# Optimization experiments

Measured on AMD Instinct MI355X. Metric: run time of the kernel, lower is better.

The kernel has to match this reference:

```python
import jax, jax.numpy as jnp
import numpy as np

D_MODEL = 512
N_HEADS = 8
HEAD_DIM = D_MODEL // N_HEADS
ROPE_BASE = 10000.0


def _rope_cache(seq_len, dtype):
    half = HEAD_DIM // 2
    inv_freq = 1.0 / (ROPE_BASE ** (jnp.arange(half, dtype=dtype) / half))
    t = jnp.arange(seq_len, dtype=dtype)
    freqs = jnp.einsum('i,j->ij', t, inv_freq)            # [L, half]
    cos = jnp.repeat(jnp.cos(freqs), 2, axis=-1)          # [L, head_dim]
    sin = jnp.repeat(jnp.sin(freqs), 2, axis=-1)
    return cos[None, None], sin[None, None]               # [1,1,L,head_dim]


def _rotate_half(x):
    x_even = x[..., ::2]
    x_odd = x[..., 1::2]
    return jnp.stack([-x_odd, x_even], axis=-1).reshape(x.shape)


def setup_inputs() -> dict:
    key = jax.random.key(0)
    ks = jax.random.split(key, 10)
    B, Lq, Lkv, C = 2, 2048, 4096, D_MODEL
    s = 1.0 / np.sqrt(C)
    inp = {
        'q': jax.random.normal(ks[0], (B, Lq, C), jnp.float32),
        'kv': jax.random.normal(ks[1], (B, Lkv, C), jnp.float32),
        'Wq': jax.random.normal(ks[2], (C, C), jnp.float32) * s,
        'bq': jnp.zeros((C,), jnp.float32),
        'Wk': jax.random.normal(ks[3], (C, C), jnp.float32) * s,
        'bk': jnp.zeros((C,), jnp.float32),
        'Wv': jax.random.normal(ks[4], (C, C), jnp.float32) * s,
        'bv': jnp.zeros((C,), jnp.float32),
        'Wo': jax.random.normal(ks[5], (C, C), jnp.float32) * s,
        'bo': jnp.zeros((C,), jnp.float32),
    }
    return inp


def reference(q, kv, Wq, bq, Wk, bk, Wv, bv, Wo, bo):
    B, Lq, C = q.shape
    Lkv = kv.shape[1]
    H, Dh = N_HEADS, HEAD_DIM
    # projections (torch Linear: x @ W.T + b)
    qh = (q @ Wq.T + bq).reshape(B, Lq, H, Dh).transpose(0, 2, 1, 3)    # [B,H,Lq,Dh]
    kh = (kv @ Wk.T + bk).reshape(B, Lkv, H, Dh).transpose(0, 2, 1, 3)  # [B,H,Lkv,Dh]
    vh = (kv @ Wv.T + bv).reshape(B, Lkv, H, Dh).transpose(0, 2, 1, 3)
    # RoPE applied to K only
    cos, sin = _rope_cache(Lkv, kh.dtype)
    kh = kh * cos + _rotate_half(kh) * sin
    # manual softmax attention (full [B,H,Lq,Lkv] matrix, as in the source)
    scale = 1.0 / np.sqrt(Dh).astype(np.float32)
    attn = jnp.einsum('bhqd,bhkd->bhqk', qh, kh) * scale
    attn = jax.nn.softmax(attn, axis=-1)
    out = jnp.einsum('bhqk,bhkd->bhqd', attn, vh)
    out = out.transpose(0, 2, 1, 3).reshape(B, Lq, C)
    return out @ Wo.T + bo
```

## Files before the change

kernel.cpp:

```cpp
#include <hip/hip_runtime.h>
#include <math.h>

typedef _Float16 f16;
typedef __attribute__((ext_vector_type(8))) f16 f16x8;
typedef __attribute__((ext_vector_type(4))) float f32x4;
typedef __attribute__((ext_vector_type(4))) int   i32x4;

__device__ __forceinline__ short f2h(float f) {
    return __builtin_bit_cast(short, (f16)f);
}

__device__ __forceinline__ void gload16(const void* g, void* l) {
    __builtin_amdgcn_global_load_lds(
        (const __attribute__((address_space(1))) unsigned int*)g,
        (__attribute__((address_space(3))) unsigned int*)l, 16, 0, 0);
}

#define MFMA16(A, B, C) __builtin_amdgcn_mfma_f32_16x16x32_f16(A, B, C, 0, 0, 0)
#define EXP2(x) __builtin_amdgcn_exp2f(x)

__global__ __launch_bounds__(256) void convert_kernel(
    const float* __restrict__ q, const float* __restrict__ kv,
    const float* __restrict__ Wq, const float* __restrict__ Wk,
    const float* __restrict__ Wv, const float* __restrict__ Wo,
    short* __restrict__ cq, short* __restrict__ ckv,
    short* __restrict__ wq, short* __restrict__ wk,
    short* __restrict__ wv, short* __restrict__ wo)
{
    int g = blockIdx.x * 256 + threadIdx.x;
    const float* src; short* dst; int local;
    if      (g <  524288) { src = q;  dst = cq;  local = g; }
    else if (g < 1572864) { src = kv; dst = ckv; local = g -  524288; }
    else if (g < 1638400) { src = Wq; dst = wq;  local = g - 1572864; }
    else if (g < 1703936) { src = Wk; dst = wk;  local = g - 1638400; }
    else if (g < 1769472) { src = Wv; dst = wv;  local = g - 1703936; }
    else                  { src = Wo; dst = wo;  local = g - 1769472; }
    float4 v = *(const float4*)(src + (size_t)local * 4);
    short4 hv; short* hp = (short*)&hv;
    hp[0] = f2h(v.x); hp[1] = f2h(v.y); hp[2] = f2h(v.z); hp[3] = f2h(v.w);
    *(short4*)(dst + (size_t)local * 4) = hv;
}

template<int RT, int EP>
__device__ __forceinline__ void gemm_core(
    short* As, short* Bs,
    const short* __restrict__ X, const short* __restrict__ W,
    const float* __restrict__ bias, float scale,
    float* __restrict__ outF, short* __restrict__ outH,
    int m0, int n0)
{
    const int tid  = threadIdx.x;
    const int wave = tid >> 6, lane = tid & 63;
    const int quad = lane >> 4, col = lane & 15;
    const int wy = wave >> 1, wx = wave & 1;
    constexpr int MT  = RT / 32;
    constexpr int ASZ = RT * 32;

    f32x4 acc[MT][4];
    #pragma unroll
    for (int i = 0; i < MT; ++i)
        #pragma unroll
        for (int j = 0; j < 4; ++j) acc[i][j] = (f32x4){0.f, 0.f, 0.f, 0.f};

    int aoff[MT], boff[4];
    #pragma unroll
    for (int t = 0; t < MT; ++t)
        aoff[t] = (wy * (RT / 2) + t * 16 + col) * 32 + quad * 8;
    #pragma unroll
    for (int t = 0; t < 4; ++t)
        boff[t] = (wx * 64 + t * 16 + col) * 32 + quad * 8;

    const short* Abase = X + (size_t)m0 * 512;
    const short* Bbase = W + (size_t)n0 * 512;

#define STAGE_G(BUF, KB) {                                                   \
    _Pragma("unroll")                                                        \
    for (int i = 0; i < RT / 64; ++i) {                                      \
        int p = i * 256 + tid; int r = p >> 2, qq = p & 3;                   \
        gload16(Abase + (size_t)r * 512 + (KB) + qq * 8,                     \
                &As[(BUF) * ASZ + (i * 256 + wave * 64) * 8]);               \
    }                                                                        \
    _Pragma("unroll")                                                        \
    for (int i = 0; i < 2; ++i) {                                            \
        int p = i * 256 + tid; int r = p >> 2, qq = p & 3;                   \
        gload16(Bbase + (size_t)r * 512 + (KB) + qq * 8,                     \
                &Bs[(BUF) * 4096 + (i * 256 + wave * 64) * 8]);              \
    }                                                                        \
}

    STAGE_G(0, 0);
    asm volatile("s_waitcnt vmcnt(0)" ::: "memory");
    __syncthreads();

    for (int kb = 0; kb < 512; kb += 32) {
        const int cur = (kb >> 5) & 1;
        if (kb + 32 < 512) STAGE_G(cur ^ 1, kb + 32);
        f16x8 a[MT], b[4];
        #pragma unroll
        for (int t = 0; t < MT; ++t) a[t] = *(const f16x8*)&As[cur * ASZ + aoff[t]];
        #pragma unroll
        for (int t = 0; t < 4; ++t)  b[t] = *(const f16x8*)&Bs[cur * 4096 + boff[t]];
        #pragma unroll
        for (int tm = 0; tm < MT; ++tm)
            #pragma unroll
            for (int tn = 0; tn < 4; ++tn)
                acc[tm][tn] = MFMA16(a[tm], b[tn], acc[tm][tn]);
        asm volatile("s_waitcnt vmcnt(0)" ::: "memory");
        __syncthreads();
    }
#undef STAGE_G

    #pragma unroll
    for (int tn = 0; tn < 4; ++tn) {
        int ng = n0 + wx * 64 + tn * 16 + col;
        float bb = bias[ng];
        #pragma unroll
        for (int tm = 0; tm < MT; ++tm) {
            int mb = m0 + wy * (RT / 2) + tm * 16 + quad * 4;
            if constexpr (EP == 2) {
                int bb_ = mb >> 12, kvg = mb & 4095;
                int tile = kvg >> 7, kv128 = kvg & 127;
                int t01 = (kv128 >> 6) & 1, sv = (kv128 >> 4) & 3, qd = (kv128 >> 2) & 3;
                int hh = ng >> 6, dd = ng & 63, dt = dd >> 4, d15 = dd & 15;
                size_t base = ((((size_t)((bb_ * 8 + hh) * 32 + tile) * 16)
                               + sv * 4 + dt) * 64 + qd * 16 + d15) * 8 + t01 * 4;
                short4 s4; short* sp = (short*)&s4;
                #pragma unroll
                for (int r = 0; r < 4; ++r) sp[r] = f2h(acc[tm][tn][r] + bb);
                *(short4*)&outH[base] = s4;
            } else if constexpr (EP == 1) {
                #pragma unroll
                for (int r = 0; r < 4; ++r)
                    outH[(size_t)(mb + r) * 512 + ng] =
                        f2h((acc[tm][tn][r] + bb) * scale);
            } else {
                #pragma unroll
                for (int r = 0; r < 4; ++r)
                    outF[(size_t)(mb + r) * 512 + ng] = acc[tm][tn][r] + bb;
            }
        }
    }
}

__global__ __launch_bounds__(256) void fused_qkv_gemm_kernel(
    const short* __restrict__ cq, const short* __restrict__ ckv,
    const short* __restrict__ wq, const short* __restrict__ wk,
    const short* __restrict__ wv,
    const float* __restrict__ bq, const float* __restrict__ bk,
    const float* __restrict__ bv, float qscale,
    short* __restrict__ Qh, short* __restrict__ Kh, short* __restrict__ Vf)
{
    __shared__ short As[2 * 128 * 32], Bs[2 * 128 * 32];
    int bi = blockIdx.x;
    if (bi < 128) {
        gemm_core<128, 1>(As, Bs, cq, wq, bq, qscale, nullptr, Qh,
                          (bi >> 2) * 128, (bi & 3) * 128);
    } else if (bi < 384) {
        bi -= 128;
        gemm_core<128, 1>(As, Bs, ckv, wk, bk, 1.0f, nullptr, Kh,
                          (bi >> 2) * 128, (bi & 3) * 128);
    } else {
        bi -= 384;
        gemm_core<128, 2>(As, Bs, ckv, wv, bv, 1.0f, nullptr, Vf,
                          (bi >> 2) * 128, (bi & 3) * 128);
    }
}

__global__ __launch_bounds__(256) void gemm_o_kernel(
    const short* __restrict__ X, const short* __restrict__ W,
    const float* __restrict__ bias, float* __restrict__ outF)
{
    __shared__ short As[2 * 64 * 32], Bs[2 * 128 * 32];
    gemm_core<64, 0>(As, Bs, X, W, bias, 1.0f, outF, nullptr,
                     (int)(blockIdx.x >> 2) * 64, (int)(blockIdx.x & 3) * 128);
}

__global__ __launch_bounds__(256) void rope_kernel(short* __restrict__ Kh)
{
    __shared__ float2 tbl[4][32];
    const int t = threadIdx.x;
    const int g = blockIdx.x * 256 + t;
    if (t < 128) {
        int p = t >> 5, i = t & 31;
        int pos = (blockIdx.x * 4 + p) & 4095;
        float fr = expf((float)i * -0.28782313662425576f);
        float sv, cv;
        sincosf((float)pos * fr, &sv, &cv);
        tbl[p][i] = make_float2(cv, sv);
    }
    __syncthreads();

    int row = g >> 6;
    int c8  = (g & 63) * 8;
    size_t off = (size_t)row * 512 + c8;
    f16x8 hv = *(const f16x8*)&Kh[off];
    float x[8];
    #pragma unroll
    for (int j = 0; j < 8; ++j) x[j] = (float)hv[j];
    const int rl = row & 3;
    const int ib = (c8 & 63) >> 1;
    #pragma unroll
    for (int p = 0; p < 4; ++p) {
        float2 cs = tbl[rl][ib + p];
        float e = x[2 * p], o = x[2 * p + 1];
        x[2 * p]     = e * cs.x - o * cs.y;
        x[2 * p + 1] = o * cs.x + e * cs.y;
    }
    #pragma unroll
    for (int j = 0; j < 8; ++j) hv[j] = (f16)x[j];
    *(f16x8*)&Kh[off] = hv;
}

__global__ __launch_bounds__(256, 2) void attn_mfma_kernel(
    const short* __restrict__ Qh, const short* __restrict__ Kh,
    const short* __restrict__ Vfrag, short* __restrict__ AO)
{
    __shared__ char smem[17408];

    const int tid  = threadIdx.x;
    const int wave = tid >> 6;
    const int lane = tid & 63;
    const int quad = lane >> 4;
    const int l15  = lane & 15;

    const int bh = blockIdx.x & 15;
    const int qt = blockIdx.x >> 4;
    const int b  = bh >> 3, h = bh & 7;
    const int qb = qt * 32;

    f16x8 qf[2][2];
    #pragma unroll
    for (int tq = 0; tq < 2; ++tq)
        #pragma unroll
        for (int c = 0; c < 2; ++c)
            qf[tq][c] = *(const f16x8*)&Qh[((size_t)(b * 2048 + qb + tq * 16 + l15)) * 512
                                           + h * 64 + c * 32 + quad * 8];

    f32x4 o[2][4];
    f32x4 l4[2];
    #pragma unroll
    for (int i = 0; i < 2; ++i) {
        l4[i] = (f32x4){0.f, 0.f, 0.f, 0.f};
        #pragma unroll
        for (int j = 0; j < 4; ++j) o[i][j] = (f32x4){0.f, 0.f, 0.f, 0.f};
    }

    const f32x4 zero4 = (f32x4){0.f, 0.f, 0.f, 0.f};
    f16x8 vones;
    #pragma unroll
    for (int j = 0; j < 8; ++j) vones[j] = (f16)1.0f;

    const short* kp = Kh + ((size_t)(b * 4096 + wave * 16 + l15)) * 512
                      + h * 64 + quad * 8;
    const short* vbase = Vfrag + (size_t)(b * 8 + h) * 262144
                         + ((size_t)(wave * 4) * 64 + lane) * 8;

#define LDK(DST, I) { const short* _k = kp + (size_t)(I) * 65536;            \
    DST[0] = *(const f16x8*)(_k);                                            \
    DST[1] = *(const f16x8*)(_k + 32);                                       \
    DST[2] = *(const f16x8*)(_k + 32768);                                    \
    DST[3] = *(const f16x8*)(_k + 32800); }
#define LDV(DST, I) { const short* _v = vbase + (size_t)(I) * 8192;          \
    DST[0] = *(const f16x8*)(_v);                                            \
    DST[1] = *(const f16x8*)(_v + 512);                                      \
    DST[2] = *(const f16x8*)(_v + 1024);                                     \
    DST[3] = *(const f16x8*)(_v + 1536); }

#define QK(KC) {                                                             \
    __builtin_amdgcn_s_setprio(1);                                           \
    _Pragma("unroll")                                                        \
    for (int t = 0; t < 2; ++t) {                                            \
        s0[t] = MFMA16(KC[0], qf[t][0], zero4);                              \
        s0[t] = MFMA16(KC[1], qf[t][1], s0[t]);                              \
        s1[t] = MFMA16(KC[2], qf[t][0], zero4);                              \
        s1[t] = MFMA16(KC[3], qf[t][1], s1[t]);                              \
    }                                                                        \
    __builtin_amdgcn_s_setprio(0); }

#define FIN(VP) {                                                            \
    _Pragma("unroll")                                                        \
    for (int t = 0; t < 2; ++t) {                                            \
        float e0 = EXP2(s0[t][0]), e1 = EXP2(s0[t][1]);                      \
        float e2 = EXP2(s0[t][2]), e3 = EXP2(s0[t][3]);                      \
        float e4 = EXP2(s1[t][0]), e5 = EXP2(s1[t][1]);                      \
        float e6 = EXP2(s1[t][2]), e7 = EXP2(s1[t][3]);                      \
        i32x4 pw;                                                            \
        pw.x = __builtin_bit_cast(int, __builtin_amdgcn_cvt_pkrtz(e0, e1));  \
        pw.y = __builtin_bit_cast(int, __builtin_amdgcn_cvt_pkrtz(e2, e3));  \
        pw.z = __builtin_bit_cast(int, __builtin_amdgcn_cvt_pkrtz(e4, e5));  \
        pw.w = __builtin_bit_cast(int, __builtin_amdgcn_cvt_pkrtz(e6, e7));  \
        f16x8 p8 = __builtin_bit_cast(f16x8, pw);                            \
        __builtin_amdgcn_s_setprio(1);                                       \
        _Pragma("unroll")                                                    \
        for (int dt = 0; dt < 4; ++dt)                                       \
            o[t][dt] = MFMA16(p8, VP[dt], o[t][dt]);                         \
        l4[t] = MFMA16(p8, vones, l4[t]);                                    \
        __builtin_amdgcn_s_setprio(0);                                       \
    } }

    f16x8 kK[4], vV[4];
    f32x4 s0[2], s1[2];

    LDV(vV, 0);
    LDK(kK, 0);
    QK(kK);

    #pragma unroll 1
    for (int it = 1; it < 32; ++it) {
        LDK(kK, it);
        FIN(vV);
        LDV(vV, it);
        QK(kK);
    }
    FIN(vV);

#undef FIN
#undef QK
#undef LDV
#undef LDK

    float* Opart = (float*)smem;
    float* Lpart = (float*)(smem + 16896);

    float inv_save[4];
    #pragma unroll
    for (int pass = 0; pass < 2; ++pass) {
        if (pass) __syncthreads();
        #pragma unroll
        for (int tq = 0; tq < 2; ++tq)
            #pragma unroll
            for (int dh = 0; dh < 2; ++dh) {
                int dt = pass * 2 + dh;
                #pragma unroll
                for (int r = 0; r < 4; ++r)
                    Opart[wave * (32 * 33) + (tq * 16 + quad * 4 + r) * 33 + dh * 16 + l15] = o[tq][dt][r];
            }
        if (pass == 0 && l15 == 0) {
            #pragma unroll
            for (int tq = 0; tq < 2; ++tq)
                #pragma unroll
                for (int r = 0; r < 4; ++r)
                    Lpart[wave * 32 + tq * 16 + quad * 4 + r] = l4[tq][r];
        }
        __syncthreads();
        #pragma unroll
        for (int r = 0; r < 4; ++r) {
            int qq = wave * 8 + r * 2 + (lane >> 5);
            int d  = lane & 31;
            float v = Opart[0 * (32 * 33) + qq * 33 + d] + Opart[1 * (32 * 33) + qq * 33 + d]
                    + Opart[2 * (32 * 33) + qq * 33 + d] + Opart[3 * (32 * 33) + qq * 33 + d];
            float inv;
            if (pass == 0) {
                float l = Lpart[qq] + Lpart[32 + qq] + Lpart[64 + qq] + Lpart[96 + qq];
                inv = 1.0f / l;
                inv_save[r] = inv;
            } else {
                inv = inv_save[r];
            }
            float val = v * inv;
            size_t oo = ((size_t)(b * 2048 + qb + qq)) * 512 + h * 64 + pass * 32 + d;
            AO[oo] = f2h(val);
        }
    }
}

extern "C" void kernel_launch(void* const* d_in, const int* in_sizes, int n_in,
                              void* d_out, int out_size, void* d_ws, size_t ws_size,
                              hipStream_t stream) {
    const float* q  = (const float*)d_in[0];
    const float* kv = (const float*)d_in[1];
    const float* Wq = (const float*)d_in[2];
    const float* bq = (const float*)d_in[3];
    const float* Wk = (const float*)d_in[4];
    const float* bk = (const float*)d_in[5];
    const float* Wv = (const float*)d_in[6];
    const float* bv = (const float*)d_in[7];
    const float* Wo = (const float*)d_in[8];
    const float* bo = (const float*)d_in[9];
    float* out = (float*)d_out;

    char* ws = (char*)d_ws;
    const size_t MB = 1024 * 1024;
    short* cq  = (short*)(ws + 0 * MB);
    short* ckv = (short*)(ws + 4 * MB);
    short* wq  = (short*)(ws + 12 * MB);
    short* wk  = wq + 262144;
    short* wv  = wk + 262144;
    short* wo  = wv + 262144;
    short* Qh  = (short*)(ws + 14 * MB);
    short* Kh  = (short*)(ws + 18 * MB);
    short* Vf  = (short*)(ws + 26 * MB);
    short* AO  = (short*)(ws + 34 * MB);

    const float qscale = 0.18033688011112043f;

    dim3 blk(256);
    convert_kernel<<<7168, blk, 0, stream>>>(
        q, kv, Wq, Wk, Wv, Wo, cq, ckv, wq, wk, wv, wo);

    fused_qkv_gemm_kernel<<<640, blk, 0, stream>>>(
        cq, ckv, wq, wk, wv, bq, bk, bv, qscale, Qh, Kh, Vf);

    rope_kernel<<<2048, blk, 0, stream>>>(Kh);

    attn_mfma_kernel<<<1024, blk, 0, stream>>>(Qh, Kh, Vf, AO);

    gemm_o_kernel<<<256, blk, 0, stream>>>(AO, wo, bo, out);
}
```

Measured before the change: 197.3 us.

## Double-buffer K/V fragments, compute row sums in VALU, raise occupancy

The K and V register fragments are now double-buffered, so the loads for the next tile are issued a full iteration ahead of use, with the loop unrolled by two. The row-sum MFMA against a ones vector is replaced by scalar adds of the exponentials plus a cross-lane shuffle reduction, which removes one MFMA per tile. Launch bounds are raised to three blocks per SIMD pair to increase occupancy. The extra buffers raise register pressure, and the tighter register budget may cause spills.

```diff
diff --git a/kernel.cpp b/kernel.cpp
--- a/kernel.cpp
+++ b/kernel.cpp
@@ -211,7 +211,7 @@
     *(f16x8*)&Kh[off] = hv;
 }
 
-__global__ __launch_bounds__(256, 2) void attn_mfma_kernel(
+__global__ __launch_bounds__(256, 3) void attn_mfma_kernel(
     const short* __restrict__ Qh, const short* __restrict__ Kh,
     const short* __restrict__ Vfrag, short* __restrict__ AO)
 {
@@ -237,18 +237,13 @@
                                            + h * 64 + c * 32 + quad * 8];
 
     f32x4 o[2][4];
-    f32x4 l4[2];
-    #pragma unroll
-    for (int i = 0; i < 2; ++i) {
-        l4[i] = (f32x4){0.f, 0.f, 0.f, 0.f};
+    float lsum[2] = {0.f, 0.f};
+    #pragma unroll
+    for (int i = 0; i < 2; ++i)
         #pragma unroll
         for (int j = 0; j < 4; ++j) o[i][j] = (f32x4){0.f, 0.f, 0.f, 0.f};
-    }
 
     const f32x4 zero4 = (f32x4){0.f, 0.f, 0.f, 0.f};
-    f16x8 vones;
-    #pragma unroll
-    for (int j = 0; j < 8; ++j) vones[j] = (f16)1.0f;
 
     const short* kp = Kh + ((size_t)(b * 4096 + wave * 16 + l15)) * 512
                       + h * 64 + quad * 8;
@@ -284,6 +279,7 @@
         float e2 = EXP2(s0[t][2]), e3 = EXP2(s0[t][3]);                      \
         float e4 = EXP2(s1[t][0]), e5 = EXP2(s1[t][1]);                      \
         float e6 = EXP2(s1[t][2]), e7 = EXP2(s1[t][3]);                      \
+        lsum[t] += ((e0 + e1) + (e2 + e3)) + ((e4 + e5) + (e6 + e7));        \
         i32x4 pw;                                                            \
         pw.x = __builtin_bit_cast(int, __builtin_amdgcn_cvt_pkrtz(e0, e1));  \
         pw.y = __builtin_bit_cast(int, __builtin_amdgcn_cvt_pkrtz(e2, e3));  \
@@ -294,30 +290,40 @@
         _Pragma("unroll")                                                    \
         for (int dt = 0; dt < 4; ++dt)                                       \
             o[t][dt] = MFMA16(p8, VP[dt], o[t][dt]);                         \
-        l4[t] = MFMA16(p8, vones, l4[t]);                                    \
         __builtin_amdgcn_s_setprio(0);                                       \
     } }
 
-    f16x8 kK[4], vV[4];
+#define BODY(I, KC, KN, VP) {                                                \
+    LDK(KN, (I) + 1);                                                        \
+    FIN(VP);                                                                 \
+    LDV(VP, (I) + 1);                                                        \
+    QK(KC); }
+
+    f16x8 kA[4], kB[4], vA[4], vB[4];
     f32x4 s0[2], s1[2];
 
-    LDV(vV, 0);
-    LDK(kK, 0);
-    QK(kK);
+    LDK(kA, 0); LDV(vA, 0); LDK(kB, 1); LDV(vB, 1);
+    QK(kA);
 
     #pragma unroll 1
-    for (int it = 1; it < 32; ++it) {
-        LDK(kK, it);
-        FIN(vV);
-        LDV(vV, it);
-        QK(kK);
-    }
-    FIN(vV);
-
+    for (int j = 1; j < 31; j += 2) {
+        BODY(j,     kB, kA, vA);
+        BODY(j + 1, kA, kB, vB);
+    }
+    BODY(31, kB, kA, vA);
+    FIN(vB);
+
+#undef BODY
 #undef FIN
 #undef QK
 #undef LDV
 #undef LDK
+
+    #pragma unroll
+    for (int t = 0; t < 2; ++t) {
+        lsum[t] += __shfl_xor(lsum[t], 16);
+        lsum[t] += __shfl_xor(lsum[t], 32);
+    }
 
     float* Opart = (float*)smem;
     float* Lpart = (float*)(smem + 16896);
@@ -335,12 +341,9 @@
                 for (int r = 0; r < 4; ++r)
                     Opart[wave * (32 * 33) + (tq * 16 + quad * 4 + r) * 33 + dh * 16 + l15] = o[tq][dt][r];
             }
-        if (pass == 0 && l15 == 0) {
-            #pragma unroll
-            for (int tq = 0; tq < 2; ++tq)
-                #pragma unroll
-                for (int r = 0; r < 4; ++r)
-                    Lpart[wave * 32 + tq * 16 + quad * 4 + r] = l4[tq][r];
+        if (pass == 0 && quad == 0) {
+            Lpart[wave * 32 + l15]      = lsum[0];
+            Lpart[wave * 32 + 16 + l15] = lsum[1];
         }
         __syncthreads();
         #pragma unroll
```

Measured after the change: 279.3 us. 41.6% more time.

## Stage K tiles through LDS with async global_load_lds double buffering

Applied to the files above, without the earlier changes.

K fragments for the attention QK step are now fetched asynchronously straight into per-wave LDS double buffers with global_load_lds and read back from LDS just before the MFMAs. V fragments are double-buffered in registers across an unrolled-by-two loop. Explicit s_waitcnt vmcnt counts control when data is ready. The aim is to hide global load latency behind the exp/PV work and reduce register pressure from K prefetch. The trade-offs are more LDS use and fragile hand-counted waits. The final iteration also issues loads for a nonexistent 33rd tile, which reads past the end of the K and V buffers.

```diff
diff --git a/kernel.cpp b/kernel.cpp
--- a/kernel.cpp
+++ b/kernel.cpp
@@ -215,7 +215,7 @@
     const short* __restrict__ Qh, const short* __restrict__ Kh,
     const short* __restrict__ Vfrag, short* __restrict__ AO)
 {
-    __shared__ char smem[17408];
+    __shared__ char smem[32768];
 
     const int tid  = threadIdx.x;
     const int wave = tid >> 6;
@@ -255,25 +255,34 @@
     const short* vbase = Vfrag + (size_t)(b * 8 + h) * 262144
                          + ((size_t)(wave * 4) * 64 + lane) * 8;
 
-#define LDK(DST, I) { const short* _k = kp + (size_t)(I) * 65536;            \
-    DST[0] = *(const f16x8*)(_k);                                            \
-    DST[1] = *(const f16x8*)(_k + 32);                                       \
-    DST[2] = *(const f16x8*)(_k + 32768);                                    \
-    DST[3] = *(const f16x8*)(_k + 32800); }
+    short* sw = (short*)smem + wave * 4096;
+
+#define STG(I, P) { const short* _k = kp + (size_t)(I) * 65536;              \
+    short* _d = sw + (P) * 2048;                                             \
+    gload16(_k,              _d);                                            \
+    gload16(_k + 32,         _d + 512);                                      \
+    gload16(_k + 32768,      _d + 1024);                                     \
+    gload16(_k + 32768 + 32, _d + 1536); }
+
 #define LDV(DST, I) { const short* _v = vbase + (size_t)(I) * 8192;          \
     DST[0] = *(const f16x8*)(_v);                                            \
     DST[1] = *(const f16x8*)(_v + 512);                                      \
     DST[2] = *(const f16x8*)(_v + 1024);                                     \
     DST[3] = *(const f16x8*)(_v + 1536); }
 
-#define QK(KC) {                                                             \
+#define QKL(P) {                                                             \
+    const short* _kb = sw + (P) * 2048;                                      \
+    f16x8 k0 = *(const f16x8*)(_kb + lane * 8);                              \
+    f16x8 k1 = *(const f16x8*)(_kb + 512 + lane * 8);                        \
+    f16x8 k2 = *(const f16x8*)(_kb + 1024 + lane * 8);                       \
+    f16x8 k3 = *(const f16x8*)(_kb + 1536 + lane * 8);                       \
     __builtin_amdgcn_s_setprio(1);                                           \
     _Pragma("unroll")                                                        \
     for (int t = 0; t < 2; ++t) {                                            \
-        s0[t] = MFMA16(KC[0], qf[t][0], zero4);                              \
-        s0[t] = MFMA16(KC[1], qf[t][1], s0[t]);                              \
-        s1[t] = MFMA16(KC[2], qf[t][0], zero4);                              \
-        s1[t] = MFMA16(KC[3], qf[t][1], s1[t]);                              \
+        s0[t] = MFMA16(k0, qf[t][0], zero4);                                 \
+        s0[t] = MFMA16(k1, qf[t][1], s0[t]);                                 \
+        s1[t] = MFMA16(k2, qf[t][0], zero4);                                 \
+        s1[t] = MFMA16(k3, qf[t][1], s1[t]);                                 \
     }                                                                        \
     __builtin_amdgcn_s_setprio(0); }
 
@@ -298,26 +307,36 @@
         __builtin_amdgcn_s_setprio(0);                                       \
     } }
 
-    f16x8 kK[4], vV[4];
+#define BODY(I, VP) {                                                        \
+    STG((I) + 1, ((I) + 1) & 1);                                             \
+    FIN(VP);                                                                 \
+    LDV(VP, (I) + 1);                                                        \
+    asm volatile("s_waitcnt vmcnt(8)" ::: "memory");                         \
+    QKL((I) & 1); }
+
+    f16x8 vA[4], vB[4];
     f32x4 s0[2], s1[2];
 
-    LDV(vV, 0);
-    LDK(kK, 0);
-    QK(kK);
+    STG(0, 0); LDV(vA, 0); STG(1, 1); LDV(vB, 1);
+    asm volatile("s_waitcnt vmcnt(12)" ::: "memory");
+    QKL(0);
 
     #pragma unroll 1
-    for (int it = 1; it < 32; ++it) {
-        LDK(kK, it);
-        FIN(vV);
-        LDV(vV, it);
-        QK(kK);
-    }
-    FIN(vV);
-
+    for (int j = 1; j < 31; j += 2) {
+        BODY(j,     vA);
+        BODY(j + 1, vB);
+    }
+    BODY(31, vA);
+    FIN(vB);
+
+#undef BODY
 #undef FIN
-#undef QK
+#undef QKL
 #undef LDV
-#undef LDK
+#undef STG
+
+    asm volatile("s_waitcnt vmcnt(0)" ::: "memory");
+    __syncthreads();
 
     float* Opart = (float*)smem;
     float* Lpart = (float*)(smem + 16896);
```

Measured after the change: 202.1 us. 1.02x slower.
